# Optimization experiments

Hardware: AMD Instinct MI355X
Metric: run time of the kernel (lower is better)

Reference implementation:

```python
import jax, jax.numpy as jnp
import numpy as np

B, H, W = 8, 56, 56
DIM_IN = 1792 + 2   # concatenated pyramid channels + 2 coord channels
D_OUT = 1792 // 4   # gamma_d = 4
N_CENTERS = H * W   # gamma_c = 1
K = 3


def avg_pool3(x):
    # F.avg_pool2d(x, 3, 1, 1) with count_include_pad=True: padded sum / 9
    s = jax.lax.reduce_window(x, 0.0, jax.lax.add, (1, 1, 3, 3), (1, 1, 1, 1),
                              ((0, 0), (0, 0), (1, 1), (1, 1)))
    return s / 9.0


def setup_inputs() -> dict:
    key = jax.random.key(0)
    k0, k1, k2, kw, kb, kc = jax.random.split(key, 6)
    p0 = jax.random.normal(k0, (B, 256, H, W), dtype=jnp.float32)
    p1 = jax.random.normal(k1, (B, 512, 28, 28), dtype=jnp.float32)
    p2 = jax.random.normal(k2, (B, 1024, 14, 14), dtype=jnp.float32)
    conv_w = jax.random.normal(kw, (D_OUT, DIM_IN), dtype=jnp.float32) * 0.02
    conv_b = jax.random.normal(kb, (D_OUT,), dtype=jnp.float32) * 0.01
    C = jax.random.normal(kc, (D_OUT, N_CENTERS), dtype=jnp.float32) * 0.5
    return {"p0": p0, "p1": p1, "p2": p2, "conv_w": conv_w, "conv_b": conv_b, "C": C}


def reference(p0, p1, p2, conv_w, conv_b, C):
    # Descriptor: avg-pool each level, upsample to first level, concat channels
    o0 = avg_pool3(p0)
    o1 = avg_pool3(p1)
    o2 = avg_pool3(p2)
    o1 = jax.image.resize(o1, (B, o1.shape[1], H, W), method='bilinear')  # align_corners=False equiv (upsample)
    o2 = jax.image.resize(o2, (B, o2.shape[1], H, W), method='bilinear')
    sample = jnp.concatenate([o0, o1, o2], axis=1)  # (B, 1792, H, W)

    # AddCoords: xx = row index / (H-1), yy = col index / (W-1), both *2-1
    xx = (jnp.arange(H, dtype=jnp.float32) / (H - 1) * 2 - 1)[:, None] * jnp.ones((1, W), jnp.float32)
    yy = (jnp.arange(W, dtype=jnp.float32) / (W - 1) * 2 - 1)[None, :] * jnp.ones((H, 1), jnp.float32)
    coords = jnp.broadcast_to(jnp.stack([xx, yy])[None], (B, 2, H, W))
    sample = jnp.concatenate([sample, coords], axis=1)  # (B, 1794, H, W)

    # 1x1 CoordConv
    phi = jnp.einsum('bchw,oc->bohw', sample, conv_w) + conv_b[None, :, None, None]
    phi_p = phi.transpose(0, 2, 3, 1).reshape(B, H * W, D_OUT)  # b (h w) c

    # squared distance to center bank via norm expansion
    feat2 = jnp.sum(phi_p ** 2, axis=2, keepdims=True)        # (B, HW, 1)
    cent2 = jnp.sum(C ** 2, axis=0)[None, None, :]            # (1, 1, N)
    dist = jnp.sqrt(feat2 + cent2 - 2.0 * jnp.matmul(phi_p, C))  # (B, HW, N)

    # top-K smallest, ascending
    neg_top, _ = jax.lax.top_k(-dist, K)
    topv = -neg_top                                           # (B, HW, K) ascending
    soft = jax.nn.softmax(-topv, axis=-1)                     # softmin
    score = soft[:, :, 0] * topv[:, :, 0]                     # (B, HW)
    return score.reshape(B, 1, H, W)
```

## Files before the change

kernel.cpp:

```cpp
#include <hip/hip_runtime.h>
#include <math.h>

#define B_    8
#define H_    56
#define W_    56
#define HW_   3136
#define C0_   256
#define C1_   512
#define C2_   1024
#define DIN_  1794
#define KD_   1792
#define KCP_  56
#define DOUT_ 448
#define NCHP_ 28
#define NC_   3136
#define NCHD_ 196
#define KCD_  14
#define DTS_  452
#define PCH_  28672

typedef __attribute__((ext_vector_type(8))) short bh8;
typedef __attribute__((ext_vector_type(4))) float f32x4;

__device__ __forceinline__ short f2bf(float f) {
  union { float f; unsigned u; } v; v.f = f;
  unsigned r = v.u + 0x7fffu + ((v.u >> 16) & 1u);
  return (short)(r >> 16);
}
__device__ __forceinline__ float bf2f(short s) {
  union { unsigned u; float f; } v; v.u = ((unsigned)(unsigned short)s) << 16;
  return v.f;
}

__global__ __launch_bounds__(256) void desc0_kernel(const float* __restrict__ p0,
                                                    short* __restrict__ desc) {
  __shared__ float sv[64 * 57];
  const int c0 = blockIdx.x * 64, h = blockIdx.y, b = blockIdx.z;
  for (int item = threadIdx.x; item < 64 * 56; item += 256) {
    int x = item % 56, c = item / 56;
    const float* src = p0 + (((size_t)(b * C0_ + c0 + c)) * 56 + h) * 56 + x;
    float s = src[0];
    if (h > 0)  s += src[-56];
    if (h < 55) s += src[56];
    sv[c * 57 + x] = s;
  }
  __syncthreads();
  for (int item = threadIdx.x; item < 56 * 8; item += 256) {
    int g = item & 7, w = item >> 3;
    bh8 o;
#pragma unroll
    for (int j = 0; j < 8; ++j) {
      const float* s0 = sv + (g * 8 + j) * 57;
      float v = s0[w];
      if (w > 0)  v += s0[w - 1];
      if (w < 55) v += s0[w + 1];
      o[j] = f2bf(v * (1.0f / 9.0f));
    }
    size_t pid = (size_t)b * HW_ + h * 56 + w;
    *(bh8*)(desc + pid * KD_ + c0 + g * 8) = o;
  }
}

__global__ __launch_bounds__(256) void desc1_kernel(const float* __restrict__ p1,
                                                    short* __restrict__ desc) {
  __shared__ float sv[2 * 64 * 29];
  const int c0 = blockIdx.x * 64, h = blockIdx.y, b = blockIdx.z;
  float sy = (h + 0.5f) * 0.5f - 0.5f;
  float fyf = floorf(sy);
  float fy = sy - fyf;
  int iy = (int)fyf;
  int pya = min(max(iy, 0), 27), pyb = min(max(iy + 1, 0), 27);
  for (int item = threadIdx.x; item < 64 * 2 * 28; item += 256) {
    int x = item % 28;
    int pr = (item / 28) & 1;
    int c = item / 56;
    int r = pr ? pyb : pya;
    const float* src = p1 + (((size_t)(b * C1_ + c0 + c)) * 28 + r) * 28 + x;
    float s = src[0];
    if (r > 0)  s += src[-28];
    if (r < 27) s += src[28];
    sv[pr * (64 * 29) + c * 29 + x] = s;
  }
  __syncthreads();
  for (int item = threadIdx.x; item < 56 * 8; item += 256) {
    int g = item & 7, w = item >> 3;
    float sx = (w + 0.5f) * 0.5f - 0.5f;
    float fxf = floorf(sx);
    float fx = sx - fxf;
    int ix = (int)fxf;
    int x0 = min(max(ix, 0), 27), x1 = min(max(ix + 1, 0), 27);
    bh8 o;
#pragma unroll
    for (int j = 0; j < 8; ++j) {
      const float* s0 = sv + (g * 8 + j) * 29;
      const float* s1 = s0 + 64 * 29;
      float p00 = s0[x0] + (x0 > 0 ? s0[x0 - 1] : 0.f) + (x0 < 27 ? s0[x0 + 1] : 0.f);
      float p01 = s0[x1] + (x1 > 0 ? s0[x1 - 1] : 0.f) + (x1 < 27 ? s0[x1 + 1] : 0.f);
      float p10 = s1[x0] + (x0 > 0 ? s1[x0 - 1] : 0.f) + (x0 < 27 ? s1[x0 + 1] : 0.f);
      float p11 = s1[x1] + (x1 > 0 ? s1[x1 - 1] : 0.f) + (x1 < 27 ? s1[x1 + 1] : 0.f);
      float top = p00 + fx * (p01 - p00);
      float bot = p10 + fx * (p11 - p10);
      o[j] = f2bf((top + fy * (bot - top)) * (1.0f / 9.0f));
    }
    size_t pid = (size_t)b * HW_ + h * 56 + w;
    *(bh8*)(desc + pid * KD_ + C0_ + c0 + g * 8) = o;
  }
}

__global__ __launch_bounds__(256) void desc2_kernel(const float* __restrict__ p2,
                                                    short* __restrict__ desc) {
  __shared__ float sv[2 * 64 * 15];
  const int c0 = blockIdx.x * 64, h = blockIdx.y, b = blockIdx.z;
  float sy = (h + 0.5f) * 0.25f - 0.5f;
  float fyf = floorf(sy);
  float fy = sy - fyf;
  int iy = (int)fyf;
  int pya = min(max(iy, 0), 13), pyb = min(max(iy + 1, 0), 13);
  for (int item = threadIdx.x; item < 64 * 2 * 14; item += 256) {
    int x = item % 14;
    int pr = (item / 14) & 1;
    int c = item / 28;
    int r = pr ? pyb : pya;
    const float* src = p2 + (((size_t)(b * C2_ + c0 + c)) * 14 + r) * 14 + x;
    float s = src[0];
    if (r > 0)  s += src[-14];
    if (r < 13) s += src[14];
    sv[pr * (64 * 15) + c * 15 + x] = s;
  }
  __syncthreads();
  for (int item = threadIdx.x; item < 56 * 8; item += 256) {
    int g = item & 7, w = item >> 3;
    float sx = (w + 0.5f) * 0.25f - 0.5f;
    float fxf = floorf(sx);
    float fx = sx - fxf;
    int ix = (int)fxf;
    int x0 = min(max(ix, 0), 13), x1 = min(max(ix + 1, 0), 13);
    bh8 o;
#pragma unroll
    for (int j = 0; j < 8; ++j) {
      const float* s0 = sv + (g * 8 + j) * 15;
      const float* s1 = s0 + 64 * 15;
      float p00 = s0[x0] + (x0 > 0 ? s0[x0 - 1] : 0.f) + (x0 < 13 ? s0[x0 + 1] : 0.f);
      float p01 = s0[x1] + (x1 > 0 ? s0[x1 - 1] : 0.f) + (x1 < 13 ? s0[x1 + 1] : 0.f);
      float p10 = s1[x0] + (x0 > 0 ? s1[x0 - 1] : 0.f) + (x0 < 13 ? s1[x0 + 1] : 0.f);
      float p11 = s1[x1] + (x1 > 0 ? s1[x1 - 1] : 0.f) + (x1 < 13 ? s1[x1 + 1] : 0.f);
      float top = p00 + fx * (p01 - p00);
      float bot = p10 + fx * (p11 - p10);
      o[j] = f2bf((top + fy * (bot - top)) * (1.0f / 9.0f));
    }
    size_t pid = (size_t)b * HW_ + h * 56 + w;
    *(bh8*)(desc + pid * KD_ + C0_ + C1_ + c0 + g * 8) = o;
  }
}

__global__ void cent2_kernel(const float* __restrict__ C, float* __restrict__ c2) {
  int j = blockIdx.x * blockDim.x + threadIdx.x;
  if (j >= NC_) return;
  float s = 0.f;
  for (int d = 0; d < DOUT_; ++d) {
    float v = bf2f(f2bf(C[(size_t)d * NC_ + j]));
    s = fmaf(v, v, s);
  }
  c2[j] = s;
}

__global__ void cpack_kernel(const float* __restrict__ C, short* __restrict__ Cpk) {
  int idx = blockIdx.x * 256 + threadIdx.x;
  int ln = idx & 63;
  int kc = (idx >> 6) % KCD_;
  int nc = idx / (KCD_ * 64);
  int n  = nc * 16 + (ln & 15);
  int k0 = kc * 32 + ((ln >> 4) << 3);
  bh8 o;
#pragma unroll
  for (int j = 0; j < 8; ++j) o[j] = f2bf(C[(size_t)(k0 + j) * NC_ + n]);
  *(bh8*)(Cpk + (size_t)idx * 8) = o;
}

__global__ void wpack_kernel(const float* __restrict__ W, short* __restrict__ Wpk) {
  int idx = blockIdx.x * 256 + threadIdx.x;
  int ln = idx & 63;
  int kc = (idx >> 6) % KCP_;
  int nc = idx / (KCP_ * 64);
  int n  = nc * 16 + (ln & 15);
  int k0 = kc * 32 + ((ln >> 4) << 3);
  bh8 o;
#pragma unroll
  for (int j = 0; j < 8; ++j) o[j] = f2bf(W[(size_t)n * DIN_ + k0 + j]);
  *(bh8*)(Wpk + (size_t)idx * 8) = o;
}

__global__ __launch_bounds__(256) void phi_mfma(
    const short* __restrict__ desc, const short* __restrict__ Wpk,
    const float* __restrict__ cw, const float* __restrict__ cb,
    short* __restrict__ phip ) {
  __shared__ __align__(16) float Dt[16 * DTS_];
  const int wv = threadIdx.x >> 6, ln = threadIdx.x & 63;
  const int pix0 = blockIdx.x * 32;
  const short* aptr = desc + ((size_t)(pix0 + (ln & 15))) * KD_ + ((ln >> 4) << 3);

  f32x4 acc[2][7];
#pragma unroll
  for (int rc = 0; rc < 2; ++rc)
#pragma unroll
    for (int i = 0; i < 7; ++i) acc[rc][i] = (f32x4){0.f, 0.f, 0.f, 0.f};

  const short* bbase = Wpk + (size_t)(wv * 7) * (KCP_ * 512) + ln * 8;
  for (int kc = 0; kc < KCP_; ++kc) {
    bh8 a0 = *(const bh8*)(aptr + kc * 32);
    bh8 a1 = *(const bh8*)(aptr + 16 * KD_ + kc * 32);
    const short* bp = bbase + kc * 512;
#pragma unroll
    for (int i = 0; i < 7; ++i) {
      bh8 bfr = *(const bh8*)(bp + (size_t)i * (KCP_ * 512));
      acc[0][i] = __builtin_amdgcn_mfma_f32_16x16x32_bf16(a0, bfr, acc[0][i], 0, 0, 0);
      acc[1][i] = __builtin_amdgcn_mfma_f32_16x16x32_bf16(a1, bfr, acc[1][i], 0, 0, 0);
    }
  }

  for (int rc = 0; rc < 2; ++rc) {
    __syncthreads();
#pragma unroll
    for (int i = 0; i < 7; ++i) {
      int col = (wv * 7 + i) * 16 + (ln & 15);
      float bias = cb[col];
      float wx = cw[(size_t)col * DIN_ + 1792];
      float wy = cw[(size_t)col * DIN_ + 1793];
#pragma unroll
      for (int r = 0; r < 4; ++r) {
        int row = ((ln >> 4) << 2) + r;
        int pid = pix0 + rc * 16 + row;
        int hw = pid % HW_;
        int hh = hw / 56, ww = hw % 56;
        float xx = (float)hh * (2.0f / 55.0f) - 1.0f;
        float yy = (float)ww * (2.0f / 55.0f) - 1.0f;
        Dt[row * DTS_ + col] = acc[rc][i][r] + bias + wx * xx + wy * yy;
      }
    }
    __syncthreads();
    short* op = phip + (size_t)(blockIdx.x * 2 + rc) * PCH_;
    for (int item = threadIdx.x; item < KCD_ * 64; item += 256) {
      int kc = item >> 6, lp = item & 63;
      int m = lp & 15, k0 = kc * 32 + ((lp >> 4) << 3);
      bh8 o;
#pragma unroll
      for (int j = 0; j < 8; ++j) o[j] = f2bf(Dt[m * DTS_ + k0 + j]);
      *(bh8*)(op + (size_t)item * 8) = o;
    }
  }
}

__device__ __forceinline__ void insert3(float& t0, float& t1, float& t2, float v) {
  if (v < t2) {
    if (v < t1) {
      t2 = t1;
      if (v < t0) { t1 = t0; t0 = v; } else t1 = v;
    } else t2 = v;
  }
}
__device__ __forceinline__ void merge3(float& a0, float& a1, float& a2,
                                       float b0, float b1, float b2) {
  float lo0 = fminf(a0, b0), hi0 = fmaxf(a0, b0);
  float lo1 = fminf(a1, b1), hi1 = fmaxf(a1, b1);
  float lo2 = fminf(a2, b2);
  a0 = lo0;
  a1 = fminf(hi0, lo1);
  a2 = fminf(fmaxf(hi0, lo1), fminf(hi1, lo2));
}
__device__ __forceinline__ float sumsq8(bh8 a, float s) {
#pragma unroll
  for (int j = 0; j < 8; ++j) { float v = bf2f(a[j]); s = fmaf(v, v, s); }
  return s;
}

#define AFRAG_LIST(X) X(0) X(1) X(2) X(3) X(4) X(5) X(6) X(7) X(8) X(9) X(10) X(11) X(12) X(13)

__global__ __launch_bounds__(256, 4) void dist_part(
    const short* __restrict__ phip, const short* __restrict__ Cpk,
    const float* __restrict__ c2g, float* __restrict__ part) {
  const int wv = threadIdx.x >> 6, ln = threadIdx.x & 63;
  const int chunk = blockIdx.x * 2 + (wv >> 1);
  const int half  = wv & 1;

  const short* ap = phip + (size_t)chunk * PCH_ + ln * 8;
#define LOADA(i) bh8 A##i = *(const bh8*)(ap + (i) * 512);
  AFRAG_LIST(LOADA)
#undef LOADA

  float sum = 0.f;
#define SQ(i) sum = sumsq8(A##i, sum);
  AFRAG_LIST(SQ)
#undef SQ
  sum += __shfl_xor(sum, 16, 64);
  sum += __shfl_xor(sum, 32, 64);
  const int rb = (ln >> 4) << 2;
  float f2r0 = __shfl(sum, rb + 0, 64);
  float f2r1 = __shfl(sum, rb + 1, 64);
  float f2r2 = __shfl(sum, rb + 2, 64);
  float f2r3 = __shfl(sum, rb + 3, 64);

  float t00 = 1e30f, t01 = 1e30f, t02 = 1e30f;
  float t10 = 1e30f, t11 = 1e30f, t12 = 1e30f;
  float t20 = 1e30f, t21 = 1e30f, t22 = 1e30f;
  float t30 = 1e30f, t31 = 1e30f, t32 = 1e30f;

  const int nc0 = half * (NCHD_ / 2);
  const short* bbase = Cpk + (size_t)nc0 * (KCD_ * 512) + ln * 8;
  const float* c2base = c2g + (size_t)nc0 * 16 + (ln & 15);
  for (int i = 0; i < NCHD_ / 4; ++i) {
    const short* bpA = bbase + (size_t)(2 * i) * (KCD_ * 512);
    const short* bpB = bpA + (KCD_ * 512);
    f32x4 accA = {0.f, 0.f, 0.f, 0.f}, accB = {0.f, 0.f, 0.f, 0.f};
#define MF(kc) { \
    bh8 bA = *(const bh8*)(bpA + (kc) * 512); \
    bh8 bB = *(const bh8*)(bpB + (kc) * 512); \
    accA = __builtin_amdgcn_mfma_f32_16x16x32_bf16(A##kc, bA, accA, 0, 0, 0); \
    accB = __builtin_amdgcn_mfma_f32_16x16x32_bf16(A##kc, bB, accB, 0, 0, 0); }
    AFRAG_LIST(MF)
#undef MF
    float c2A = c2base[(size_t)(2 * i) * 16];
    float c2B = c2base[(size_t)(2 * i + 1) * 16];
    insert3(t00, t01, t02, f2r0 + c2A - 2.0f * accA[0]);
    insert3(t10, t11, t12, f2r1 + c2A - 2.0f * accA[1]);
    insert3(t20, t21, t22, f2r2 + c2A - 2.0f * accA[2]);
    insert3(t30, t31, t32, f2r3 + c2A - 2.0f * accA[3]);
    insert3(t00, t01, t02, f2r0 + c2B - 2.0f * accB[0]);
    insert3(t10, t11, t12, f2r1 + c2B - 2.0f * accB[1]);
    insert3(t20, t21, t22, f2r2 + c2B - 2.0f * accB[2]);
    insert3(t30, t31, t32, f2r3 + c2B - 2.0f * accB[3]);
  }

#pragma unroll
  for (int m = 1; m <= 8; m <<= 1) {
    float b0, b1, b2;
    b0 = __shfl_xor(t00, m, 64); b1 = __shfl_xor(t01, m, 64); b2 = __shfl_xor(t02, m, 64);
    merge3(t00, t01, t02, b0, b1, b2);
    b0 = __shfl_xor(t10, m, 64); b1 = __shfl_xor(t11, m, 64); b2 = __shfl_xor(t12, m, 64);
    merge3(t10, t11, t12, b0, b1, b2);
    b0 = __shfl_xor(t20, m, 64); b1 = __shfl_xor(t21, m, 64); b2 = __shfl_xor(t22, m, 64);
    merge3(t20, t21, t22, b0, b1, b2);
    b0 = __shfl_xor(t30, m, 64); b1 = __shfl_xor(t31, m, 64); b2 = __shfl_xor(t32, m, 64);
    merge3(t30, t31, t32, b0, b1, b2);
  }

  if ((ln & 15) == 0) {
    float* q = part + ((size_t)(chunk * 16 + rb)) * 8 + half * 4;
    q[0] = t00; q[1] = t01; q[2] = t02;
    q[8] = t10; q[9] = t11; q[10] = t12;
    q[16] = t20; q[17] = t21; q[18] = t22;
    q[24] = t30; q[25] = t31; q[26] = t32;
  }
}

__global__ __launch_bounds__(256) void merge_kernel(const float* __restrict__ part,
                                                    float* __restrict__ out) {
  int p = blockIdx.x * 256 + threadIdx.x;
  const float* q = part + (size_t)p * 8;
  float a0 = q[0], a1 = q[1], a2 = q[2];
  merge3(a0, a1, a2, q[4], q[5], q[6]);
  float d0 = sqrtf(fmaxf(a0, 0.f));
  float d1 = sqrtf(fmaxf(a1, 0.f));
  float d2 = sqrtf(fmaxf(a2, 0.f));
  float s0 = 1.0f / (1.0f + expf(d0 - d1) + expf(d0 - d2));
  out[p] = s0 * d0;
}

extern "C" void kernel_launch(void* const* d_in, const int* in_sizes, int n_in,
                              void* d_out, int out_size, void* d_ws, size_t ws_size,
                              hipStream_t stream) {
  const float* p0 = (const float*)d_in[0];
  const float* p1 = (const float*)d_in[1];
  const float* p2 = (const float*)d_in[2];
  const float* cw = (const float*)d_in[3];
  const float* cb = (const float*)d_in[4];
  const float* C  = (const float*)d_in[5];
  float* out = (float*)d_out;

  short* desc = (short*)d_ws;
  short* Cpk  = desc + (size_t)25088 * KD_;
  short* Wpk  = Cpk + (size_t)NCHD_ * KCD_ * 512;
  float* c2   = (float*)(Wpk + (size_t)NCHP_ * KCP_ * 512);
  float* part = c2 + NC_;

  desc0_kernel<<<dim3(4, 56, 8),  256, 0, stream>>>(p0, desc);
  desc1_kernel<<<dim3(8, 56, 8),  256, 0, stream>>>(p1, desc);
  desc2_kernel<<<dim3(16, 56, 8), 256, 0, stream>>>(p2, desc);
  cent2_kernel<<<(NC_ + 255) / 256, 256, 0, stream>>>(C, c2);
  cpack_kernel<<<NCHD_ * KCD_ * 64 / 256, 256, 0, stream>>>(C, Cpk);
  wpack_kernel<<<NCHP_ * KCP_ * 64 / 256, 256, 0, stream>>>(cw, Wpk);
  phi_mfma<<<25088 / 32, 256, 0, stream>>>(desc, Wpk, cw, cb, desc);
  dist_part<<<25088 / 32, 256, 0, stream>>>(desc, Cpk, c2, part);
  merge_kernel<<<25088 / 256, 256, 0, stream>>>(part, out);
}
```

Before: 680.7 us.

## Stage center bank tiles in LDS via async global_load_lds double buffering

The distance kernel now has all four waves of a block share one quarter of the center bank, which is streamed into shared memory with double-buffered direct global-to-LDS loads. Before, each wave read its own B fragments from global memory. The center bank is padded to 200 chunks, with sentinel norms of 1e30, so it splits evenly into quarters. The partial top-3 buffer grows to four slots per pixel and the merge kernel combines all four. The aim is to cut redundant global/L2 traffic for C and hide load latency; the cost is a barrier per step, more blocks, and an occupancy hint of two waves per EU.

```diff
diff --git a/kernel.cpp b/kernel.cpp
--- a/kernel.cpp
+++ b/kernel.cpp
@@ -15,9 +15,12 @@
 #define NCHP_ 28
 #define NC_   3136
 #define NCHD_ 196
+#define NCPAD_ 200
+#define QCH_  50
 #define KCD_  14
 #define DTS_  452
 #define PCH_  28672
+#define CHS_  7168
 
 typedef __attribute__((ext_vector_type(8))) short bh8;
 typedef __attribute__((ext_vector_type(4))) float f32x4;
@@ -155,7 +158,8 @@
 
 __global__ void cent2_kernel(const float* __restrict__ C, float* __restrict__ c2) {
   int j = blockIdx.x * blockDim.x + threadIdx.x;
-  if (j >= NC_) return;
+  if (j >= NCPAD_ * 16) return;
+  if (j >= NC_) { c2[j] = 1e30f; return; }
   float s = 0.f;
   for (int d = 0; d < DOUT_; ++d) {
     float v = bf2f(f2bf(C[(size_t)d * NC_ + j]));
@@ -173,7 +177,7 @@
   int k0 = kc * 32 + ((ln >> 4) << 3);
   bh8 o;
 #pragma unroll
-  for (int j = 0; j < 8; ++j) o[j] = f2bf(C[(size_t)(k0 + j) * NC_ + n]);
+  for (int j = 0; j < 8; ++j) o[j] = (n < NC_) ? f2bf(C[(size_t)(k0 + j) * NC_ + n]) : (short)0;
   *(bh8*)(Cpk + (size_t)idx * 8) = o;
 }
 
@@ -275,12 +279,15 @@
 
 #define AFRAG_LIST(X) X(0) X(1) X(2) X(3) X(4) X(5) X(6) X(7) X(8) X(9) X(10) X(11) X(12) X(13)
 
-__global__ __launch_bounds__(256, 4) void dist_part(
-    const short* __restrict__ phip, const short* __restrict__ Cpk,
-    const float* __restrict__ c2g, float* __restrict__ part) {
+__global__ __launch_bounds__(256) __attribute__((amdgpu_waves_per_eu(2, 2)))
+void dist_part(const short* __restrict__ phip, const short* __restrict__ Cpk,
+               const float* __restrict__ c2g, float* __restrict__ part) {
+  __shared__ __align__(16) short sB[2][2 * CHS_];
   const int wv = threadIdx.x >> 6, ln = threadIdx.x & 63;
-  const int chunk = blockIdx.x * 2 + (wv >> 1);
-  const int half  = wv & 1;
+  const int pg = blockIdx.x >> 2;
+  const int quarter = blockIdx.x & 3;
+  const int chunk = pg * 4 + wv;
+  const int nc0 = quarter * QCH_;
 
   const short* ap = phip + (size_t)chunk * PCH_ + ln * 8;
 #define LOADA(i) bh8 A##i = *(const bh8*)(ap + (i) * 512);
@@ -304,22 +311,43 @@
   float t20 = 1e30f, t21 = 1e30f, t22 = 1e30f;
   float t30 = 1e30f, t31 = 1e30f, t32 = 1e30f;
 
-  const int nc0 = half * (NCHD_ / 2);
-  const short* bbase = Cpk + (size_t)nc0 * (KCD_ * 512) + ln * 8;
+  const short* csrc = Cpk + (size_t)nc0 * CHS_;
   const float* c2base = c2g + (size_t)nc0 * 16 + (ln & 15);
-  for (int i = 0; i < NCHD_ / 4; ++i) {
-    const short* bpA = bbase + (size_t)(2 * i) * (KCD_ * 512);
-    const short* bpB = bpA + (KCD_ * 512);
+
+#pragma unroll
+  for (int c = 0; c < 7; ++c) {
+    int slot = wv * 7 + c;
+    __builtin_amdgcn_global_load_lds(
+        (const __attribute__((address_space(1))) unsigned int*)(csrc + slot * 512 + ln * 8),
+        (__attribute__((address_space(3))) unsigned int*)(&sB[0][slot * 512]),
+        16, 0, 0);
+  }
+
+  for (int p = 0; p < 25; ++p) {
+    __syncthreads();
+    if (p + 1 < 25) {
+      const short* src = csrc + (size_t)(p + 1) * (2 * CHS_);
+#pragma unroll
+      for (int c = 0; c < 7; ++c) {
+        int slot = wv * 7 + c;
+        __builtin_amdgcn_global_load_lds(
+            (const __attribute__((address_space(1))) unsigned int*)(src + slot * 512 + ln * 8),
+            (__attribute__((address_space(3))) unsigned int*)(&sB[(p + 1) & 1][slot * 512]),
+            16, 0, 0);
+      }
+    }
+    const short* bufA = &sB[p & 1][0] + ln * 8;
+    const short* bufB = bufA + CHS_;
     f32x4 accA = {0.f, 0.f, 0.f, 0.f}, accB = {0.f, 0.f, 0.f, 0.f};
 #define MF(kc) { \
-    bh8 bA = *(const bh8*)(bpA + (kc) * 512); \
-    bh8 bB = *(const bh8*)(bpB + (kc) * 512); \
+    bh8 bA = *(const bh8*)(bufA + (kc) * 512); \
+    bh8 bB = *(const bh8*)(bufB + (kc) * 512); \
     accA = __builtin_amdgcn_mfma_f32_16x16x32_bf16(A##kc, bA, accA, 0, 0, 0); \
     accB = __builtin_amdgcn_mfma_f32_16x16x32_bf16(A##kc, bB, accB, 0, 0, 0); }
     AFRAG_LIST(MF)
 #undef MF
-    float c2A = c2base[(size_t)(2 * i) * 16];
-    float c2B = c2base[(size_t)(2 * i + 1) * 16];
+    float c2A = c2base[(size_t)(2 * p) * 16];
+    float c2B = c2base[(size_t)(2 * p + 1) * 16];
     insert3(t00, t01, t02, f2r0 + c2A - 2.0f * accA[0]);
     insert3(t10, t11, t12, f2r1 + c2A - 2.0f * accA[1]);
     insert3(t20, t21, t22, f2r2 + c2A - 2.0f * accA[2]);
@@ -344,20 +372,21 @@
   }
 
   if ((ln & 15) == 0) {
-    float* q = part + ((size_t)(chunk * 16 + rb)) * 8 + half * 4;
-    q[0] = t00; q[1] = t01; q[2] = t02;
-    q[8] = t10; q[9] = t11; q[10] = t12;
-    q[16] = t20; q[17] = t21; q[18] = t22;
-    q[24] = t30; q[25] = t31; q[26] = t32;
+    float* qp = part + ((size_t)(chunk * 16 + rb)) * 16 + quarter * 4;
+    qp[0]  = t00; qp[1]  = t01; qp[2]  = t02;
+    qp[16] = t10; qp[17] = t11; qp[18] = t12;
+    qp[32] = t20; qp[33] = t21; qp[34] = t22;
+    qp[48] = t30; qp[49] = t31; qp[50] = t32;
   }
 }
 
 __global__ __launch_bounds__(256) void merge_kernel(const float* __restrict__ part,
                                                     float* __restrict__ out) {
   int p = blockIdx.x * 256 + threadIdx.x;
-  const float* q = part + (size_t)p * 8;
+  const float* q = part + (size_t)p * 16;
   float a0 = q[0], a1 = q[1], a2 = q[2];
-  merge3(a0, a1, a2, q[4], q[5], q[6]);
+#pragma unroll
+  for (int w = 1; w < 4; ++w) merge3(a0, a1, a2, q[w * 4], q[w * 4 + 1], q[w * 4 + 2]);
   float d0 = sqrtf(fmaxf(a0, 0.f));
   float d1 = sqrtf(fmaxf(a1, 0.f));
   float d2 = sqrtf(fmaxf(a2, 0.f));
@@ -378,17 +407,17 @@
 
   short* desc = (short*)d_ws;
   short* Cpk  = desc + (size_t)25088 * KD_;
-  short* Wpk  = Cpk + (size_t)NCHD_ * KCD_ * 512;
+  short* Wpk  = Cpk + (size_t)NCPAD_ * KCD_ * 512;
   float* c2   = (float*)(Wpk + (size_t)NCHP_ * KCP_ * 512);
-  float* part = c2 + NC_;
+  float* part = c2 + NCPAD_ * 16;
 
   desc0_kernel<<<dim3(4, 56, 8),  256, 0, stream>>>(p0, desc);
   desc1_kernel<<<dim3(8, 56, 8),  256, 0, stream>>>(p1, desc);
   desc2_kernel<<<dim3(16, 56, 8), 256, 0, stream>>>(p2, desc);
-  cent2_kernel<<<(NC_ + 255) / 256, 256, 0, stream>>>(C, c2);
-  cpack_kernel<<<NCHD_ * KCD_ * 64 / 256, 256, 0, stream>>>(C, Cpk);
+  cent2_kernel<<<(NCPAD_ * 16 + 255) / 256, 256, 0, stream>>>(C, c2);
+  cpack_kernel<<<NCPAD_ * KCD_ * 64 / 256, 256, 0, stream>>>(C, Cpk);
   wpack_kernel<<<NCHP_ * KCP_ * 64 / 256, 256, 0, stream>>>(cw, Wpk);
   phi_mfma<<<25088 / 32, 256, 0, stream>>>(desc, Wpk, cw, cb, desc);
-  dist_part<<<25088 / 32, 256, 0, stream>>>(desc, Cpk, c2, part);
+  dist_part<<<1568, 256, 0, stream>>>(desc, Cpk, c2, part);
   merge_kernel<<<25088 / 256, 256, 0, stream>>>(part, out);
 }
```

After: 736.7 us. +8.2%, slower.

## Split center bank across four waves per row chunk in distance kernel

Applied to the files above, without the earlier changes.

The distance/top-k kernel now assigns one 16-row chunk per block, with each of the four waves scanning a quarter of the center bank (padded from 196 to 200 chunks with dummy centers at 1e30 norm) instead of two chunks per block split in halves. This doubles the block count and halves per-wave work, aiming for better occupancy and more latency hiding. The four A-fragment loads per block are shared across waves via L1/L2 rather than replicated per pair. The merge kernel now combines four partial top-3 lists instead of two, and the partial buffer doubles in size.

```diff
diff --git a/kernel.cpp b/kernel.cpp
--- a/kernel.cpp
+++ b/kernel.cpp
@@ -15,9 +15,12 @@
 #define NCHP_ 28
 #define NC_   3136
 #define NCHD_ 196
+#define NCPAD_ 200
+#define QCH_  50
 #define KCD_  14
 #define DTS_  452
 #define PCH_  28672
+#define CHS_  7168
 
 typedef __attribute__((ext_vector_type(8))) short bh8;
 typedef __attribute__((ext_vector_type(4))) float f32x4;
@@ -155,7 +158,8 @@
 
 __global__ void cent2_kernel(const float* __restrict__ C, float* __restrict__ c2) {
   int j = blockIdx.x * blockDim.x + threadIdx.x;
-  if (j >= NC_) return;
+  if (j >= NCPAD_ * 16) return;
+  if (j >= NC_) { c2[j] = 1e30f; return; }
   float s = 0.f;
   for (int d = 0; d < DOUT_; ++d) {
     float v = bf2f(f2bf(C[(size_t)d * NC_ + j]));
@@ -173,7 +177,7 @@
   int k0 = kc * 32 + ((ln >> 4) << 3);
   bh8 o;
 #pragma unroll
-  for (int j = 0; j < 8; ++j) o[j] = f2bf(C[(size_t)(k0 + j) * NC_ + n]);
+  for (int j = 0; j < 8; ++j) o[j] = (n < NC_) ? f2bf(C[(size_t)(k0 + j) * NC_ + n]) : (short)0;
   *(bh8*)(Cpk + (size_t)idx * 8) = o;
 }
 
@@ -279,8 +283,8 @@
     const short* __restrict__ phip, const short* __restrict__ Cpk,
     const float* __restrict__ c2g, float* __restrict__ part) {
   const int wv = threadIdx.x >> 6, ln = threadIdx.x & 63;
-  const int chunk = blockIdx.x * 2 + (wv >> 1);
-  const int half  = wv & 1;
+  const int chunk = blockIdx.x;
+  const int nc0 = wv * QCH_;
 
   const short* ap = phip + (size_t)chunk * PCH_ + ln * 8;
 #define LOADA(i) bh8 A##i = *(const bh8*)(ap + (i) * 512);
@@ -304,12 +308,11 @@
   float t20 = 1e30f, t21 = 1e30f, t22 = 1e30f;
   float t30 = 1e30f, t31 = 1e30f, t32 = 1e30f;
 
-  const int nc0 = half * (NCHD_ / 2);
-  const short* bbase = Cpk + (size_t)nc0 * (KCD_ * 512) + ln * 8;
+  const short* bbase = Cpk + (size_t)nc0 * CHS_ + ln * 8;
   const float* c2base = c2g + (size_t)nc0 * 16 + (ln & 15);
-  for (int i = 0; i < NCHD_ / 4; ++i) {
-    const short* bpA = bbase + (size_t)(2 * i) * (KCD_ * 512);
-    const short* bpB = bpA + (KCD_ * 512);
+  for (int i = 0; i < QCH_ / 2; ++i) {
+    const short* bpA = bbase + (size_t)(2 * i) * CHS_;
+    const short* bpB = bpA + CHS_;
     f32x4 accA = {0.f, 0.f, 0.f, 0.f}, accB = {0.f, 0.f, 0.f, 0.f};
 #define MF(kc) { \
     bh8 bA = *(const bh8*)(bpA + (kc) * 512); \
@@ -344,20 +347,21 @@
   }
 
   if ((ln & 15) == 0) {
-    float* q = part + ((size_t)(chunk * 16 + rb)) * 8 + half * 4;
-    q[0] = t00; q[1] = t01; q[2] = t02;
-    q[8] = t10; q[9] = t11; q[10] = t12;
-    q[16] = t20; q[17] = t21; q[18] = t22;
-    q[24] = t30; q[25] = t31; q[26] = t32;
+    float* qp = part + ((size_t)(chunk * 16 + rb)) * 16 + wv * 4;
+    qp[0]  = t00; qp[1]  = t01; qp[2]  = t02;
+    qp[16] = t10; qp[17] = t11; qp[18] = t12;
+    qp[32] = t20; qp[33] = t21; qp[34] = t22;
+    qp[48] = t30; qp[49] = t31; qp[50] = t32;
   }
 }
 
 __global__ __launch_bounds__(256) void merge_kernel(const float* __restrict__ part,
                                                     float* __restrict__ out) {
   int p = blockIdx.x * 256 + threadIdx.x;
-  const float* q = part + (size_t)p * 8;
+  const float* q = part + (size_t)p * 16;
   float a0 = q[0], a1 = q[1], a2 = q[2];
-  merge3(a0, a1, a2, q[4], q[5], q[6]);
+#pragma unroll
+  for (int w = 1; w < 4; ++w) merge3(a0, a1, a2, q[w * 4], q[w * 4 + 1], q[w * 4 + 2]);
   float d0 = sqrtf(fmaxf(a0, 0.f));
   float d1 = sqrtf(fmaxf(a1, 0.f));
   float d2 = sqrtf(fmaxf(a2, 0.f));
@@ -378,17 +382,17 @@
 
   short* desc = (short*)d_ws;
   short* Cpk  = desc + (size_t)25088 * KD_;
-  short* Wpk  = Cpk + (size_t)NCHD_ * KCD_ * 512;
+  short* Wpk  = Cpk + (size_t)NCPAD_ * KCD_ * 512;
   float* c2   = (float*)(Wpk + (size_t)NCHP_ * KCP_ * 512);
-  float* part = c2 + NC_;
+  float* part = c2 + NCPAD_ * 16;
 
   desc0_kernel<<<dim3(4, 56, 8),  256, 0, stream>>>(p0, desc);
   desc1_kernel<<<dim3(8, 56, 8),  256, 0, stream>>>(p1, desc);
   desc2_kernel<<<dim3(16, 56, 8), 256, 0, stream>>>(p2, desc);
-  cent2_kernel<<<(NC_ + 255) / 256, 256, 0, stream>>>(C, c2);
-  cpack_kernel<<<NCHD_ * KCD_ * 64 / 256, 256, 0, stream>>>(C, Cpk);
+  cent2_kernel<<<(NCPAD_ * 16 + 255) / 256, 256, 0, stream>>>(C, c2);
+  cpack_kernel<<<NCPAD_ * KCD_ * 64 / 256, 256, 0, stream>>>(C, Cpk);
   wpack_kernel<<<NCHP_ * KCP_ * 64 / 256, 256, 0, stream>>>(cw, Wpk);
   phi_mfma<<<25088 / 32, 256, 0, stream>>>(desc, Wpk, cw, cb, desc);
-  dist_part<<<25088 / 32, 256, 0, stream>>>(desc, Cpk, c2, part);
+  dist_part<<<25088 / 16, 256, 0, stream>>>(desc, Cpk, c2, part);
   merge_kernel<<<25088 / 256, 256, 0, stream>>>(part, out);
 }
```

Result: no change. 689.7 us (+1.3%).
